# Kernel optimization log

Hardware: AMD Instinct MI355X
Metric: run time of the kernel (lower is better)

The kernel has to match this reference:

```python
import jax, jax.numpy as jnp
import numpy as np

N = 16384      # nodes
E = 262144     # edges
H = 512        # hidden_dim
G = 256        # graphs in batch
L = 4          # num_layers - 1 conv layers
OUT = 128      # output_dim
AF, AV = 9, 128   # atom features, atom vocab per feature
BF, BV = 3, 8     # bond features, bond vocab per feature


def setup_inputs() -> dict:
    key = jax.random.key(0)
    ks = jax.random.split(key, 10)
    h_node = jax.random.randint(ks[0], (N, AF), 0, 119, dtype=jnp.int32)
    h_edge = jax.random.randint(ks[1], (E, BF), 0, 5, dtype=jnp.int32)
    src = jax.random.randint(ks[2], (E,), 0, N, dtype=jnp.int32)
    dst = jax.random.randint(ks[3], (E,), 0, N, dtype=jnp.int32)
    gid = jnp.sort(jax.random.randint(ks[4], (N,), 0, G, dtype=jnp.int32))
    atom_emb = jax.random.normal(ks[5], (AF, AV, H), dtype=jnp.float32) * 0.02
    bond_emb = jax.random.normal(ks[6], (L, BF, BV, H), dtype=jnp.float32) * 0.02
    W = jax.random.normal(ks[7], (L, H, H), dtype=jnp.float32) / np.float32(np.sqrt(H))
    b = jnp.zeros((L, H), jnp.float32)
    gn_w = jnp.ones((L, H), jnp.float32)
    gn_b = jnp.zeros((L, H), jnp.float32)
    gn_ms = jnp.ones((L, H), jnp.float32)  # GraphNorm mean_scale (alpha)
    Wp = jax.random.normal(ks[8], (H, OUT), dtype=jnp.float32) / np.float32(np.sqrt(H))
    bp = jnp.zeros((OUT,), jnp.float32)
    return dict(h_node=h_node, h_edge=h_edge, src=src, dst=dst, gid=gid,
                atom_emb=atom_emb, bond_emb=bond_emb, W=W, b=b,
                gn_w=gn_w, gn_b=gn_b, gn_ms=gn_ms, Wp=Wp, bp=bp)


def _multi_embed_sum(tbl, idx, nfeat, vocab):
    # tbl: [nfeat, vocab, H], idx: [M, nfeat] -> sum of per-feature embeddings [M, H]
    flat = tbl.reshape(nfeat * vocab, tbl.shape[-1])
    off = idx + (jnp.arange(nfeat, dtype=idx.dtype) * vocab)[None, :]
    return flat[off].sum(axis=1)


def _graph_norm(h, gid, w, bb, ms):
    # GraphNorm: weight * (h - alpha*mean_g) / std_g + bias, per graph
    cnt = jax.ops.segment_sum(jnp.ones((h.shape[0],), h.dtype), gid, num_segments=G)
    cnt = jnp.maximum(cnt, 1.0)[:, None]
    mean = jax.ops.segment_sum(h, gid, num_segments=G) / cnt
    sub = h - mean[gid] * ms
    var = jax.ops.segment_sum(sub * sub, gid, num_segments=G) / cnt
    return w * sub / jnp.sqrt(var + 1e-6)[gid] + bb


def reference(h_node, h_edge, src, dst, gid, atom_emb, bond_emb, W, b,
              gn_w, gn_b, gn_ms, Wp, bp):
    h = _multi_embed_sum(atom_emb, h_node, AF, AV)  # AtomEncoder -> [N, H]
    ones_e = jnp.ones((E,), h.dtype)
    indeg = jnp.maximum(jax.ops.segment_sum(ones_e, dst, num_segments=N), 1.0)[:, None]
    for i in range(L):
        x = h
        he = _multi_embed_sum(bond_emb[i], h_edge, BF, BV)  # BondEncoder -> [E, H]
        msg = h[src] + he                                   # u_add_e
        neigh = jax.ops.segment_sum(msg, dst, num_segments=N) / indeg  # mean reduce
        r = h + neigh                                       # (1 + eps)*x + neigh, eps=0
        r = r @ W[i] + b[i]                                 # MLP (1-layer linear)
        r = _graph_norm(r, gid, gn_w[i], gn_b[i], gn_ms[i])
        if i != L - 1:
            r = jax.nn.relu(r)
        h = r + x                                           # residual
    pooled = jax.ops.segment_sum(h, gid, num_segments=G)    # SumPooling -> [G, H]
    return pooled @ Wp + bp                                 # [G, OUT] (dropout = eval identity)
```

## Files before the change

### kernel.cpp

```cpp
#include <hip/hip_runtime.h>

#define N_NODES 16384
#define N_EDGES 262144
#define HID 512
#define NG 256
#define NL 4
#define NOUT 128

typedef __attribute__((ext_vector_type(8))) short bf16x8;
typedef __attribute__((ext_vector_type(4))) float f32x4;
typedef __attribute__((ext_vector_type(8))) unsigned short u16x8;

static __device__ __forceinline__ unsigned short f2bf(float f) {
    unsigned int u = __float_as_uint(f);
    unsigned int r = (u + 0x7fffu + ((u >> 16) & 1u)) >> 16;
    return (unsigned short)r;
}
static __device__ __forceinline__ float bf2f(unsigned short s) {
    return __uint_as_float(((unsigned int)s) << 16);
}

static __device__ __forceinline__ void gload_lds16(const unsigned short* g, unsigned short* l) {
    __builtin_amdgcn_global_load_lds(
        (const __attribute__((address_space(1))) unsigned int*)(g),
        (__attribute__((address_space(3))) unsigned int*)(l), 16, 0, 0);
}

__global__ __launch_bounds__(256) void k_prep(const int* __restrict__ hn, const float* __restrict__ aemb,
                                              unsigned short* __restrict__ h_bf,
                                              const int* __restrict__ dst, int* __restrict__ cnt,
                                              const float* __restrict__ W, unsigned short* __restrict__ Wt,
                                              const float* __restrict__ bemb, unsigned short* __restrict__ ctab,
                                              const int* __restrict__ gid, int* __restrict__ gs,
                                              float* __restrict__ rcnt) {
    const int bid = blockIdx.x;
    const int tid = threadIdx.x;
    if (bid < 8192) {
        int n = bid * 2 + (tid >> 7);
        int c = (tid & 127) * 4;
        float4 acc = make_float4(0.f, 0.f, 0.f, 0.f);
        for (int f = 0; f < 9; ++f) {
            int v = hn[n * 9 + f];
            const float4 ev = *(const float4*)(aemb + (size_t)(f * 128 + v) * HID + c);
            acc.x += ev.x; acc.y += ev.y; acc.z += ev.z; acc.w += ev.w;
        }
        ushort4 pk;
        pk.x = f2bf(acc.x); pk.y = f2bf(acc.y); pk.z = f2bf(acc.z); pk.w = f2bf(acc.w);
        *(ushort4*)(h_bf + (size_t)n * HID + c) = pk;
    } else if (bid < 9216) {
        int e = (bid - 8192) * 256 + tid;
        atomicAdd(&cnt[dst[e]], 1);
    } else if (bid < 13312) {
        int id = (bid - 9216) * 256 + tid;
        int l = id >> 18;
        int n = (id >> 9) & 511;
        int k = id & 511;
        Wt[id] = f2bf(W[((size_t)l << 18) + ((size_t)k << 9) + n]);
    } else if (bid < 17408) {
        int id = (bid - 13312) * 256 + tid;
        int c = id & 511;
        int combo = (id >> 9) & 511;
        int l = id >> 18;
        int i0 = combo >> 6, i1 = (combo >> 3) & 7, i2 = combo & 7;
        const float* bl = bemb + (size_t)l * 3 * 8 * HID;
        float v = bl[(size_t)i0 * HID + c] + bl[(size_t)(8 + i1) * HID + c] + bl[(size_t)(16 + i2) * HID + c];
        ctab[id] = f2bf(v);
    } else {
        int g = tid;
        int lo = 0, hi = N_NODES;
        while (lo < hi) { int mid = (lo + hi) >> 1; if (gid[mid] < g) lo = mid + 1; else hi = mid; }
        gs[g] = lo;
        if (g == 0) gs[NG] = N_NODES;
        __syncthreads();
        int e = (g == NG - 1) ? N_NODES : gs[g + 1];
        rcnt[g] = 1.0f / fmaxf((float)(e - lo), 1.0f);
    }
}

__global__ void k_scan(const int* __restrict__ cnt, int* __restrict__ rs) {
    __shared__ int spre[256];
    int t = threadIdx.x;
    int base = t * 64;
    int s = 0;
    for (int i = 0; i < 64; ++i) s += cnt[base + i];
    spre[t] = s;
    __syncthreads();
    if (t == 0) {
        int run = 0;
        for (int i = 0; i < 256; ++i) { int v = spre[i]; spre[i] = run; run += v; }
        rs[N_NODES] = run;
    }
    __syncthreads();
    int run = spre[t];
    for (int i = 0; i < 64; ++i) { rs[base + i] = run; run += cnt[base + i]; }
}

__global__ void k_fillep(const int* __restrict__ dst, const int* __restrict__ rs,
                         int* __restrict__ fc, const int* __restrict__ src,
                         const int* __restrict__ hedge, int2* __restrict__ ep) {
    int e = blockIdx.x * 256 + threadIdx.x;
    int d = dst[e];
    int pos = atomicAdd(&fc[d], 1);
    int s = src[e];
    int c = hedge[e * 3 + 0] * 64 + hedge[e * 3 + 1] * 8 + hedge[e * 3 + 2];
    ep[rs[d] + pos] = make_int2(s, c);
}

#define NEDGE1(PX, PY)                                                          \
    {                                                                           \
        u16x8 a0 = *(const u16x8*)(h_bf + (size_t)(PX)*HID + c);                \
        u16x8 b0 = *(const u16x8*)(ctab + (size_t)(PY)*HID + c);                \
        _Pragma("unroll") for (int q = 0; q < 8; ++q)                           \
            acc[q] += bf2f(a0[q]) + bf2f(b0[q]);                                \
    }

__global__ __launch_bounds__(256) void k_neigh(const unsigned short* __restrict__ h_bf,
                                               const int2* __restrict__ ep,
                                               const int* __restrict__ rs,
                                               const unsigned short* __restrict__ ctab,
                                               unsigned short* __restrict__ t) {
    int n = blockIdx.x * 4 + (threadIdx.x >> 6);
    int c = (threadIdx.x & 63) * 8;
    int s = rs[n], e = rs[n + 1];
    u16x8 hself = *(const u16x8*)(h_bf + (size_t)n * HID + c);
    float acc[8] = {0.f, 0.f, 0.f, 0.f, 0.f, 0.f, 0.f, 0.f};
    int j = s;
    if (j < e && (j & 1)) {
        int2 p = ep[j];
        NEDGE1(p.x, p.y)
        ++j;
    }
    for (; j + 4 <= e; j += 4) {
        int4 pa = *(const int4*)(ep + j);
        int4 pb = *(const int4*)(ep + j + 2);
        u16x8 a0 = *(const u16x8*)(h_bf + (size_t)pa.x * HID + c);
        u16x8 b0 = *(const u16x8*)(ctab + (size_t)pa.y * HID + c);
        u16x8 a1 = *(const u16x8*)(h_bf + (size_t)pa.z * HID + c);
        u16x8 b1 = *(const u16x8*)(ctab + (size_t)pa.w * HID + c);
        u16x8 a2 = *(const u16x8*)(h_bf + (size_t)pb.x * HID + c);
        u16x8 b2 = *(const u16x8*)(ctab + (size_t)pb.y * HID + c);
        u16x8 a3 = *(const u16x8*)(h_bf + (size_t)pb.z * HID + c);
        u16x8 b3 = *(const u16x8*)(ctab + (size_t)pb.w * HID + c);
        #pragma unroll
        for (int q = 0; q < 8; ++q)
            acc[q] += ((bf2f(a0[q]) + bf2f(b0[q])) + (bf2f(a1[q]) + bf2f(b1[q])))
                    + ((bf2f(a2[q]) + bf2f(b2[q])) + (bf2f(a3[q]) + bf2f(b3[q])));
    }
    for (; j < e; ++j) {
        int2 p = ep[j];
        NEDGE1(p.x, p.y)
    }
    float inv = 1.0f / fmaxf((float)(e - s), 1.0f);
    u16x8 pk;
    #pragma unroll
    for (int q = 0; q < 8; ++q)
        pk[q] = f2bf(bf2f(hself[q]) + acc[q] * inv);
    *(u16x8*)(t + (size_t)n * HID + c) = pk;
}

#define BM 128
#define BN 64
#define BK 64

__global__ __launch_bounds__(256) void k_gemm(const unsigned short* __restrict__ A,
                                              const unsigned short* __restrict__ Bt,
                                              const float* __restrict__ bias,
                                              unsigned short* __restrict__ C) {
    __shared__ unsigned short As[BM * BK];
    __shared__ unsigned short Bs[BN * BK];
    const int tid = threadIdx.x;
    const int m0 = blockIdx.x * BM;
    const int n0 = blockIdx.y * BN;
    const int w = tid >> 6, lane = tid & 63;
    const int wm = (w >> 1) * 64, wn = (w & 1) * 32;
    const int lr = lane & 15, lg = lane >> 4;

    const int srow = tid >> 3;
    const int scol = ((tid & 7) ^ (srow & 7)) * 8;

    f32x4 acc[4][2] = {};

    for (int k0 = 0; k0 < HID; k0 += BK) {
        __syncthreads();
        #pragma unroll
        for (int r = 0; r < 4; ++r)
            gload_lds16(A + (size_t)(m0 + r * 32 + srow) * HID + k0 + scol,
                        As + r * 2048 + w * 512);
        #pragma unroll
        for (int r = 0; r < 2; ++r)
            gload_lds16(Bt + (size_t)(n0 + r * 32 + srow) * HID + k0 + scol,
                        Bs + r * 2048 + w * 512);
        __syncthreads();

        #pragma unroll
        for (int kk = 0; kk < 2; ++kk) {
            bf16x8 af[4], bfr[2];
            #pragma unroll
            for (int i = 0; i < 4; ++i) {
                int row = wm + i * 16 + lr;
                af[i] = *(const bf16x8*)(As + row * BK + (((kk * 4 + lg) ^ (row & 7)) * 8));
            }
            #pragma unroll
            for (int j = 0; j < 2; ++j) {
                int row = wn + j * 16 + lr;
                bfr[j] = *(const bf16x8*)(Bs + row * BK + (((kk * 4 + lg) ^ (row & 7)) * 8));
            }
            #pragma unroll
            for (int i = 0; i < 4; ++i)
                #pragma unroll
                for (int j = 0; j < 2; ++j)
                    acc[i][j] = __builtin_amdgcn_mfma_f32_16x16x32_bf16(af[i], bfr[j], acc[i][j], 0, 0, 0);
        }
    }

    #pragma unroll
    for (int i = 0; i < 4; ++i) {
        const int grow = m0 + wm + i * 16 + lg * 4;
        #pragma unroll
        for (int j = 0; j < 2; ++j) {
            const int gcol = n0 + wn + j * 16 + lr;
            const float bv = bias[gcol];
            #pragma unroll
            for (int rr = 0; rr < 4; ++rr)
                C[(size_t)(grow + rr) * HID + gcol] = f2bf(acc[i][j][rr] + bv);
        }
    }
}

__global__ __launch_bounds__(256) void k_gstats(const unsigned short* __restrict__ r,
                                                const int* __restrict__ gs,
                                                float* __restrict__ psum, float* __restrict__ psq) {
    int g = blockIdx.x;
    int seg = blockIdx.y;
    int s = gs[g], e = gs[g + 1];
    int c = threadIdx.x * 2;
    float s0 = 0.f, s1 = 0.f, q0 = 0.f, q1 = 0.f;
    for (int n = s + seg; n < e; n += 8) {
        ushort2 v = *(const ushort2*)(r + (size_t)n * HID + c);
        float v0 = bf2f(v.x), v1 = bf2f(v.y);
        s0 += v0; s1 += v1; q0 += v0 * v0; q1 += v1 * v1;
    }
    size_t o = ((size_t)seg * NG + g) * HID + c;
    *(float2*)(psum + o) = make_float2(s0, s1);
    *(float2*)(psq + o) = make_float2(q0, q1);
}

__global__ __launch_bounds__(256) void k_gred(const float* __restrict__ psum, const float* __restrict__ psq,
                                              float* __restrict__ gsum, float* __restrict__ gsq) {
    int idx = blockIdx.x * 256 + threadIdx.x;
    float s = 0.f, q = 0.f;
    #pragma unroll
    for (int seg = 0; seg < 8; ++seg) {
        s += psum[(size_t)seg * NG * HID + idx];
        q += psq[(size_t)seg * NG * HID + idx];
    }
    gsum[idx] = s;
    gsq[idx] = q;
}

__global__ __launch_bounds__(256) void k_gapply(const unsigned short* __restrict__ r,
                                                unsigned short* __restrict__ h_bf,
                                                const int* __restrict__ gid,
                                                const float* __restrict__ rcnt,
                                                const float* __restrict__ gsum, const float* __restrict__ gsq,
                                                const float* __restrict__ gw, const float* __restrict__ gb,
                                                const float* __restrict__ gms) {
    int n = blockIdx.x * 2 + (threadIdx.x >> 7);
    int c = (threadIdx.x & 127) * 4;
    int g = gid[n];
    float rc = rcnt[g];
    const float4 sm = *(const float4*)(gsum + (size_t)g * HID + c);
    const float4 sq = *(const float4*)(gsq + (size_t)g * HID + c);
    const float4 ms = *(const float4*)(gms + c);
    const float4 gwv = *(const float4*)(gw + c);
    const float4 gbv = *(const float4*)(gb + c);
    const ushort4 rv4 = *(const ushort4*)(r + (size_t)n * HID + c);
    const ushort4 hv4 = *(const ushort4*)(h_bf + (size_t)n * HID + c);
    float rv[4] = {bf2f(rv4.x), bf2f(rv4.y), bf2f(rv4.z), bf2f(rv4.w)};
    float hv[4] = {bf2f(hv4.x), bf2f(hv4.y), bf2f(hv4.z), bf2f(hv4.w)};
    float outv[4];
    float mean, am, var, wgt, v;
    #define CH(X, K)                                                \
        mean = sm.X * rc; am = ms.X * mean;                         \
        var = sq.X * rc - 2.f * am * mean + am * am;                \
        wgt = gwv.X * rsqrtf(var + 1e-6f);                          \
        v = (rv[K] - am) * wgt + gbv.X;                             \
        v = fmaxf(v, 0.f);                                          \
        outv[K] = v + hv[K];
    CH(x, 0)
    CH(y, 1)
    CH(z, 2)
    CH(w, 3)
    #undef CH
    ushort4 pk;
    pk.x = f2bf(outv[0]); pk.y = f2bf(outv[1]); pk.z = f2bf(outv[2]); pk.w = f2bf(outv[3]);
    *(ushort4*)(h_bf + (size_t)n * HID + c) = pk;
}

__global__ __launch_bounds__(256) void k_gpool(const unsigned short* __restrict__ r,
                                               const unsigned short* __restrict__ h_bf,
                                               const int* __restrict__ gs,
                                               const float* __restrict__ rcnt,
                                               const float* __restrict__ gsum, const float* __restrict__ gsq,
                                               const float* __restrict__ gw, const float* __restrict__ gb,
                                               const float* __restrict__ gms,
                                               float* __restrict__ ppool) {
    int g = blockIdx.x;
    int seg = blockIdx.y;
    int s = gs[g], e = gs[g + 1];
    int c = threadIdx.x * 2;
    float rc = rcnt[g];
    float2 sm = *(const float2*)(gsum + (size_t)g * HID + c);
    float2 sq = *(const float2*)(gsq + (size_t)g * HID + c);
    float2 ms = *(const float2*)(gms + c);
    float2 gwv = *(const float2*)(gw + c);
    float2 gbv = *(const float2*)(gb + c);
    float mean0 = sm.x * rc, am0 = ms.x * mean0;
    float var0 = sq.x * rc - 2.f * am0 * mean0 + am0 * am0;
    float wgt0 = gwv.x * rsqrtf(var0 + 1e-6f);
    float mean1 = sm.y * rc, am1 = ms.y * mean1;
    float var1 = sq.y * rc - 2.f * am1 * mean1 + am1 * am1;
    float wgt1 = gwv.y * rsqrtf(var1 + 1e-6f);
    float p0 = 0.f, p1 = 0.f;
    for (int n = s + seg; n < e; n += 8) {
        ushort2 rv = *(const ushort2*)(r + (size_t)n * HID + c);
        ushort2 hv = *(const ushort2*)(h_bf + (size_t)n * HID + c);
        p0 += (bf2f(rv.x) - am0) * wgt0 + gbv.x + bf2f(hv.x);
        p1 += (bf2f(rv.y) - am1) * wgt1 + gbv.y + bf2f(hv.y);
    }
    size_t o = ((size_t)seg * NG + g) * HID + c;
    *(float2*)(ppool + o) = make_float2(p0, p1);
}

__global__ __launch_bounds__(128) void k_proj(const float* __restrict__ ppool,
                                              const float* __restrict__ Wp,
                                              const float* __restrict__ bp, float* __restrict__ out) {
    int g = blockIdx.x;
    int tid = threadIdx.x;
    __shared__ float pr[HID];
    {
        int c = tid * 4;
        float4 sv = make_float4(0.f, 0.f, 0.f, 0.f);
        #pragma unroll
        for (int seg = 0; seg < 8; ++seg) {
            const float4 v = *(const float4*)(ppool + ((size_t)seg * NG + g) * HID + c);
            sv.x += v.x; sv.y += v.y; sv.z += v.z; sv.w += v.w;
        }
        *(float4*)(pr + c) = sv;
    }
    __syncthreads();
    int o = tid;
    float acc = bp[o];
    #pragma unroll 8
    for (int k = 0; k < HID; ++k) acc += pr[k] * Wp[k * NOUT + o];
    out[g * NOUT + o] = acc;
}

extern "C" void kernel_launch(void* const* d_in, const int* in_sizes, int n_in,
                              void* d_out, int out_size, void* d_ws, size_t ws_size,
                              hipStream_t stream) {
    const int*   h_node = (const int*)d_in[0];
    const int*   h_edge = (const int*)d_in[1];
    const int*   src    = (const int*)d_in[2];
    const int*   dst    = (const int*)d_in[3];
    const int*   gid    = (const int*)d_in[4];
    const float* aemb   = (const float*)d_in[5];
    const float* bemb   = (const float*)d_in[6];
    const float* W      = (const float*)d_in[7];
    const float* bias   = (const float*)d_in[8];
    const float* gnw    = (const float*)d_in[9];
    const float* gnb    = (const float*)d_in[10];
    const float* gnms   = (const float*)d_in[11];
    const float* Wp     = (const float*)d_in[12];
    const float* bp     = (const float*)d_in[13];
    float* out = (float*)d_out;

    char* ws = (char*)d_ws;
    size_t off = 0;
    auto alloc = [&](size_t bytes) -> char* {
        char* p = ws + off;
        off += (bytes + 255) & ~(size_t)255;
        return p;
    };
    int* cnt            = (int*)alloc((size_t)N_NODES * 4);
    int* fc             = (int*)alloc((size_t)N_NODES * 4);
    size_t zbytes = off;

    unsigned short* h_bf= (unsigned short*)alloc((size_t)N_NODES * HID * 2);
    unsigned short* rbf = (unsigned short*)alloc((size_t)N_NODES * HID * 2);
    unsigned short* t   = (unsigned short*)alloc((size_t)N_NODES * HID * 2);
    unsigned short* Wt  = (unsigned short*)alloc((size_t)NL * HID * HID * 2);
    unsigned short* ctab= (unsigned short*)alloc((size_t)NL * 512 * HID * 2);
    int2* ep            = (int2*)alloc((size_t)N_EDGES * 8);
    int* rs             = (int*)alloc((size_t)(N_NODES + 1) * 4);
    int* gs             = (int*)alloc((size_t)(NG + 1) * 4);
    float* rcnt         = (float*)alloc((size_t)NG * 4);
    float* pstat        = (float*)alloc((size_t)2 * 8 * NG * HID * 4);
    float* gstat        = (float*)alloc((size_t)2 * NG * HID * 4);
    float* ppool        = (float*)alloc((size_t)8 * NG * HID * 4);
    float* psum = pstat;
    float* psq  = pstat + (size_t)8 * NG * HID;
    float* gsum = gstat;
    float* gsq  = gstat + (size_t)NG * HID;

    hipMemsetAsync(cnt, 0, zbytes, stream);
    k_prep<<<17409, 256, 0, stream>>>(h_node, aemb, h_bf, dst, cnt, W, Wt, bemb, ctab,
                                      gid, gs, rcnt);
    k_scan<<<1, 256, 0, stream>>>(cnt, rs);
    k_fillep<<<N_EDGES / 256, 256, 0, stream>>>(dst, rs, fc, src, h_edge, ep);

    for (int i = 0; i < NL; ++i) {
        k_neigh<<<N_NODES / 4, 256, 0, stream>>>(h_bf, ep, rs,
                                                 ctab + (size_t)i * 512 * HID, t);
        dim3 gg(N_NODES / BM, HID / BN);
        k_gemm<<<gg, 256, 0, stream>>>(t, Wt + (size_t)i * HID * HID, bias + i * HID, rbf);
        k_gstats<<<dim3(NG, 8), 256, 0, stream>>>(rbf, gs, psum, psq);
        k_gred<<<NG * HID / 256, 256, 0, stream>>>(psum, psq, gsum, gsq);
        if (i < NL - 1) {
            k_gapply<<<N_NODES / 2, 256, 0, stream>>>(rbf, h_bf, gid, rcnt, gsum, gsq,
                                                      gnw + i * HID, gnb + i * HID, gnms + i * HID);
        } else {
            k_gpool<<<dim3(NG, 8), 256, 0, stream>>>(rbf, h_bf, gs, rcnt, gsum, gsq,
                                                     gnw + i * HID, gnb + i * HID, gnms + i * HID,
                                                     ppool);
        }
    }
    k_proj<<<NG, NOUT, 0, stream>>>(ppool, Wp, bp, out);
}
```

Baseline: 376.5 us.

## Double-buffer GEMM LDS tiles and remap neighbor-gather to column slices

The GEMM now keeps two LDS buffers and issues the global-to-LDS loads for the next K tile before computing the current one, dropping one barrier per iteration so load latency overlaps the MFMA work. Separately, the neighbor aggregation kernel is remapped so each block handles 16 nodes over a 128-column slice instead of 4 nodes over all 512 columns. Block IDs are interleaved so concurrent blocks cover different slices of the same node groups, aiming for better cache locality of the gathered rows and more edge-level parallelism per block. Double buffering doubles the GEMM's LDS use, which may lower occupancy.

```diff
diff --git a/kernel.cpp b/kernel.cpp
--- a/kernel.cpp
+++ b/kernel.cpp
@@ -119,8 +119,11 @@
                                                const int* __restrict__ rs,
                                                const unsigned short* __restrict__ ctab,
                                                unsigned short* __restrict__ t) {
-    int n = blockIdx.x * 4 + (threadIdx.x >> 6);
-    int c = (threadIdx.x & 63) * 8;
+    int bid = blockIdx.x;
+    int slice = (bid >> 1) & 3;
+    int ng = (bid >> 3) * 2 + (bid & 1);
+    int n = ng * 16 + (threadIdx.x >> 4);
+    int c = slice * 128 + (threadIdx.x & 15) * 8;
     int s = rs[n], e = rs[n + 1];
     u16x8 hself = *(const u16x8*)(h_bf + (size_t)n * HID + c);
     float acc[8] = {0.f, 0.f, 0.f, 0.f, 0.f, 0.f, 0.f, 0.f};
@@ -162,12 +165,42 @@
 #define BN 64
 #define BK 64
 
+#define GSTAGE(buf, k0)                                                           \
+    {                                                                             \
+        _Pragma("unroll") for (int r = 0; r < 4; ++r)                             \
+            gload_lds16(A + (size_t)(m0 + r * 32 + srow) * HID + (k0) + scol,     \
+                        As + (buf) * (BM * BK) + r * 2048 + w * 512);             \
+        _Pragma("unroll") for (int r = 0; r < 2; ++r)                             \
+            gload_lds16(Bt + (size_t)(n0 + r * 32 + srow) * HID + (k0) + scol,    \
+                        Bs + (buf) * (BN * BK) + r * 2048 + w * 512);             \
+    }
+
+#define GCOMP(buf)                                                                \
+    {                                                                             \
+        const unsigned short* Ab = As + (buf) * (BM * BK);                        \
+        const unsigned short* Bb = Bs + (buf) * (BN * BK);                        \
+        _Pragma("unroll") for (int kk = 0; kk < 2; ++kk) {                        \
+            bf16x8 af[4], bfr[2];                                                 \
+            _Pragma("unroll") for (int i = 0; i < 4; ++i) {                       \
+                int row = wm + i * 16 + lr;                                       \
+                af[i] = *(const bf16x8*)(Ab + row * BK + (((kk * 4 + lg) ^ (row & 7)) * 8)); \
+            }                                                                     \
+            _Pragma("unroll") for (int j = 0; j < 2; ++j) {                       \
+                int row = wn + j * 16 + lr;                                       \
+                bfr[j] = *(const bf16x8*)(Bb + row * BK + (((kk * 4 + lg) ^ (row & 7)) * 8)); \
+            }                                                                     \
+            _Pragma("unroll") for (int i = 0; i < 4; ++i)                         \
+                _Pragma("unroll") for (int j = 0; j < 2; ++j)                     \
+                    acc[i][j] = __builtin_amdgcn_mfma_f32_16x16x32_bf16(af[i], bfr[j], acc[i][j], 0, 0, 0); \
+        }                                                                         \
+    }
+
 __global__ __launch_bounds__(256) void k_gemm(const unsigned short* __restrict__ A,
                                               const unsigned short* __restrict__ Bt,
                                               const float* __restrict__ bias,
                                               unsigned short* __restrict__ C) {
-    __shared__ unsigned short As[BM * BK];
-    __shared__ unsigned short Bs[BN * BK];
+    __shared__ unsigned short As[2 * BM * BK];
+    __shared__ unsigned short Bs[2 * BN * BK];
     const int tid = threadIdx.x;
     const int m0 = blockIdx.x * BM;
     const int n0 = blockIdx.y * BN;
@@ -180,38 +213,17 @@
 
     f32x4 acc[4][2] = {};
 
-    for (int k0 = 0; k0 < HID; k0 += BK) {
+    GSTAGE(0, 0)
+    __syncthreads();
+    int cur = 0;
+    #pragma unroll
+    for (int kt = 0; kt < HID / BK - 1; ++kt) {
+        GSTAGE(cur ^ 1, (kt + 1) * BK)
+        GCOMP(cur)
         __syncthreads();
-        #pragma unroll
-        for (int r = 0; r < 4; ++r)
-            gload_lds16(A + (size_t)(m0 + r * 32 + srow) * HID + k0 + scol,
-                        As + r * 2048 + w * 512);
-        #pragma unroll
-        for (int r = 0; r < 2; ++r)
-            gload_lds16(Bt + (size_t)(n0 + r * 32 + srow) * HID + k0 + scol,
-                        Bs + r * 2048 + w * 512);
-        __syncthreads();
-
-        #pragma unroll
-        for (int kk = 0; kk < 2; ++kk) {
-            bf16x8 af[4], bfr[2];
-            #pragma unroll
-            for (int i = 0; i < 4; ++i) {
-                int row = wm + i * 16 + lr;
-                af[i] = *(const bf16x8*)(As + row * BK + (((kk * 4 + lg) ^ (row & 7)) * 8));
-            }
-            #pragma unroll
-            for (int j = 0; j < 2; ++j) {
-                int row = wn + j * 16 + lr;
-                bfr[j] = *(const bf16x8*)(Bs + row * BK + (((kk * 4 + lg) ^ (row & 7)) * 8));
-            }
-            #pragma unroll
-            for (int i = 0; i < 4; ++i)
-                #pragma unroll
-                for (int j = 0; j < 2; ++j)
-                    acc[i][j] = __builtin_amdgcn_mfma_f32_16x16x32_bf16(af[i], bfr[j], acc[i][j], 0, 0, 0);
-        }
-    }
+        cur ^= 1;
+    }
+    GCOMP(cur)
 
     #pragma unroll
     for (int i = 0; i < 4; ++i) {
@@ -410,8 +422,8 @@
     k_fillep<<<N_EDGES / 256, 256, 0, stream>>>(dst, rs, fc, src, h_edge, ep);
 
     for (int i = 0; i < NL; ++i) {
-        k_neigh<<<N_NODES / 4, 256, 0, stream>>>(h_bf, ep, rs,
-                                                 ctab + (size_t)i * 512 * HID, t);
+        k_neigh<<<4096, 256, 0, stream>>>(h_bf, ep, rs,
+                                          ctab + (size_t)i * 512 * HID, t);
         dim3 gg(N_NODES / BM, HID / BN);
         k_gemm<<<gg, 256, 0, stream>>>(t, Wt + (size_t)i * HID * HID, bias + i * HID, rbf);
         k_gstats<<<dim3(NG, 8), 256, 0, stream>>>(rbf, gs, psum, psq);
```

Result: slower. 403.5 us (+7.2%).

## Split neighbor aggregation across column slices and edge sub-groups per wave

Applied to the files above, without the earlier changes.

The neighbor-mean kernel now gives each wave a 128-column slice of a node instead of the full row. The four 16-lane groups in the wave handle interleaved edges, and their partial sums are combined with cross-lane shuffles. The grid grows fourfold, with block indices mapped so neighboring blocks cover the same nodes' different slices. This is meant to raise memory-level parallelism and occupancy for the gather, which is limited by latency on low-degree nodes. The cost is more reads of edge-list entries (each edge's pair is read once per slice) and extra shuffle work.

```diff
diff --git a/kernel.cpp b/kernel.cpp
--- a/kernel.cpp
+++ b/kernel.cpp
@@ -106,56 +106,56 @@
     ep[rs[d] + pos] = make_int2(s, c);
 }
 
-#define NEDGE1(PX, PY)                                                          \
-    {                                                                           \
-        u16x8 a0 = *(const u16x8*)(h_bf + (size_t)(PX)*HID + c);                \
-        u16x8 b0 = *(const u16x8*)(ctab + (size_t)(PY)*HID + c);                \
-        _Pragma("unroll") for (int q = 0; q < 8; ++q)                           \
-            acc[q] += bf2f(a0[q]) + bf2f(b0[q]);                                \
-    }
-
 __global__ __launch_bounds__(256) void k_neigh(const unsigned short* __restrict__ h_bf,
                                                const int2* __restrict__ ep,
                                                const int* __restrict__ rs,
                                                const unsigned short* __restrict__ ctab,
                                                unsigned short* __restrict__ t) {
-    int n = blockIdx.x * 4 + (threadIdx.x >> 6);
-    int c = (threadIdx.x & 63) * 8;
+    int bid = blockIdx.x;
+    int slice = (bid >> 1) & 3;
+    int ng = (bid >> 3) * 2 + (bid & 1);
+    int wave = threadIdx.x >> 6;
+    int lane = threadIdx.x & 63;
+    int eo = lane >> 4;
+    int cl = lane & 15;
+    int n = ng * 4 + wave;
+    int c = slice * 128 + cl * 8;
     int s = rs[n], e = rs[n + 1];
-    u16x8 hself = *(const u16x8*)(h_bf + (size_t)n * HID + c);
     float acc[8] = {0.f, 0.f, 0.f, 0.f, 0.f, 0.f, 0.f, 0.f};
-    int j = s;
-    if (j < e && (j & 1)) {
-        int2 p = ep[j];
-        NEDGE1(p.x, p.y)
-        ++j;
-    }
-    for (; j + 4 <= e; j += 4) {
-        int4 pa = *(const int4*)(ep + j);
-        int4 pb = *(const int4*)(ep + j + 2);
-        u16x8 a0 = *(const u16x8*)(h_bf + (size_t)pa.x * HID + c);
-        u16x8 b0 = *(const u16x8*)(ctab + (size_t)pa.y * HID + c);
-        u16x8 a1 = *(const u16x8*)(h_bf + (size_t)pa.z * HID + c);
-        u16x8 b1 = *(const u16x8*)(ctab + (size_t)pa.w * HID + c);
-        u16x8 a2 = *(const u16x8*)(h_bf + (size_t)pb.x * HID + c);
-        u16x8 b2 = *(const u16x8*)(ctab + (size_t)pb.y * HID + c);
-        u16x8 a3 = *(const u16x8*)(h_bf + (size_t)pb.z * HID + c);
-        u16x8 b3 = *(const u16x8*)(ctab + (size_t)pb.w * HID + c);
+    int j = s + eo;
+    for (; j + 4 < e; j += 8) {
+        int2 p0 = ep[j];
+        int2 p1 = ep[j + 4];
+        u16x8 a0 = *(const u16x8*)(h_bf + (size_t)p0.x * HID + c);
+        u16x8 b0 = *(const u16x8*)(ctab + (size_t)p0.y * HID + c);
+        u16x8 a1 = *(const u16x8*)(h_bf + (size_t)p1.x * HID + c);
+        u16x8 b1 = *(const u16x8*)(ctab + (size_t)p1.y * HID + c);
         #pragma unroll
         for (int q = 0; q < 8; ++q)
-            acc[q] += ((bf2f(a0[q]) + bf2f(b0[q])) + (bf2f(a1[q]) + bf2f(b1[q])))
-                    + ((bf2f(a2[q]) + bf2f(b2[q])) + (bf2f(a3[q]) + bf2f(b3[q])));
-    }
-    for (; j < e; ++j) {
-        int2 p = ep[j];
-        NEDGE1(p.x, p.y)
-    }
-    float inv = 1.0f / fmaxf((float)(e - s), 1.0f);
-    u16x8 pk;
+            acc[q] += (bf2f(a0[q]) + bf2f(b0[q])) + (bf2f(a1[q]) + bf2f(b1[q]));
+    }
+    if (j < e) {
+        int2 p0 = ep[j];
+        u16x8 a0 = *(const u16x8*)(h_bf + (size_t)p0.x * HID + c);
+        u16x8 b0 = *(const u16x8*)(ctab + (size_t)p0.y * HID + c);
+        #pragma unroll
+        for (int q = 0; q < 8; ++q)
+            acc[q] += bf2f(a0[q]) + bf2f(b0[q]);
+    }
     #pragma unroll
-    for (int q = 0; q < 8; ++q)
-        pk[q] = f2bf(bf2f(hself[q]) + acc[q] * inv);
-    *(u16x8*)(t + (size_t)n * HID + c) = pk;
+    for (int q = 0; q < 8; ++q) {
+        acc[q] += __shfl_xor(acc[q], 16, 64);
+        acc[q] += __shfl_xor(acc[q], 32, 64);
+    }
+    if (eo == 0) {
+        u16x8 hself = *(const u16x8*)(h_bf + (size_t)n * HID + c);
+        float inv = 1.0f / fmaxf((float)(e - s), 1.0f);
+        u16x8 pk;
+        #pragma unroll
+        for (int q = 0; q < 8; ++q)
+            pk[q] = f2bf(bf2f(hself[q]) + acc[q] * inv);
+        *(u16x8*)(t + (size_t)n * HID + c) = pk;
+    }
 }
 
 #define BM 128
@@ -410,8 +410,8 @@
     k_fillep<<<N_EDGES / 256, 256, 0, stream>>>(dst, rs, fc, src, h_edge, ep);
 
     for (int i = 0; i < NL; ++i) {
-        k_neigh<<<N_NODES / 4, 256, 0, stream>>>(h_bf, ep, rs,
-                                                 ctab + (size_t)i * 512 * HID, t);
+        k_neigh<<<16384, 256, 0, stream>>>(h_bf, ep, rs,
+                                           ctab + (size_t)i * 512 * HID, t);
         dim3 gg(N_NODES / BM, HID / BN);
         k_gemm<<<gg, 256, 0, stream>>>(t, Wt + (size_t)i * HID * HID, bias + i * HID, rbf);
         k_gstats<<<dim3(NG, 8), 256, 0, stream>>>(rbf, gs, psum, psq);
```

After: 383.4 us. Within noise of the previous version (+1.8%).
